# Kernel tuning notes

Hardware: AMD Instinct MI355X
Metric: run time of the kernel (lower is better)

Reference implementation:

```python
import jax, jax.numpy as jnp
import numpy as np

EMBED = 1024
HEAD = 64

def setup_inputs() -> dict:
    key = jax.random.key(0)
    k1, k2, k3, k4 = jax.random.split(key, 4)
    x = jax.random.normal(k1, (8, 2048, EMBED), dtype=jnp.float32)
    # nn.Linear(E, H, bias=False) weights, stored as [E, H] for x @ W
    W_k = jax.random.normal(k2, (EMBED, HEAD), dtype=jnp.float32) * (EMBED ** -0.5)
    W_q = jax.random.normal(k3, (EMBED, HEAD), dtype=jnp.float32) * (EMBED ** -0.5)
    W_v = jax.random.normal(k4, (EMBED, HEAD), dtype=jnp.float32) * (EMBED ** -0.5)
    return {"x": x, "W_k": W_k, "W_q": W_q, "W_v": W_v}

def reference(x, W_k, W_q, W_v):
    B, T, E = x.shape
    keys = jnp.einsum('bte,eh->bth', x, W_k)
    queries = jnp.einsum('bte,eh->bth', x, W_q)
    values = jnp.einsum('bte,eh->bth', x, W_v)
    # NOTE: original scales by embedding size E, not head size
    scores = jnp.einsum('bqh,bkh->bqk', queries, keys) * (E ** -0.5)
    causal = jnp.tril(jnp.ones((T, T), dtype=bool))
    scores = jnp.where(causal, scores, -jnp.inf)
    weights = jax.nn.softmax(scores, axis=-1)
    return jnp.einsum('bqk,bkh->bqh', weights, values)
```

## Files before the change

kernel.cpp:

```cpp
#include <hip/hip_runtime.h>

typedef __attribute__((ext_vector_type(8))) short bf16x8;
typedef __attribute__((ext_vector_type(4))) float f32x4;
typedef __attribute__((ext_vector_type(4))) unsigned short u16x4;
typedef __attribute__((ext_vector_type(8))) unsigned short u16x8;
typedef __attribute__((ext_vector_type(4))) unsigned int u32x4;

#define MFMA(a, b, c) __builtin_amdgcn_mfma_f32_16x16x32_bf16(a, b, c, 0, 0, 0)

static __device__ __forceinline__ unsigned short f2bf(float x) {
    union { float f; unsigned u; } v; v.f = x;
    unsigned r = v.u + 0x7fffu + ((v.u >> 16) & 1u);
    return (unsigned short)(r >> 16);
}

static __device__ __forceinline__ bf16x8 pack_pa(
    float ea0, float ea1, float ea2, float ea3,
    float eb0, float eb1, float eb2, float eb3, bool odd)
{
    unsigned a1, a2, b1, b2;
    asm("v_cvt_pk_bf16_f32 %0, %1, %2" : "=v"(a1) : "v"(ea0), "v"(ea1));
    asm("v_cvt_pk_bf16_f32 %0, %1, %2" : "=v"(a2) : "v"(ea2), "v"(ea3));
    asm("v_cvt_pk_bf16_f32 %0, %1, %2" : "=v"(b1) : "v"(eb0), "v"(eb1));
    asm("v_cvt_pk_bf16_f32 %0, %1, %2" : "=v"(b2) : "v"(eb2), "v"(eb3));
    asm("v_permlane32_swap_b32 %0, %1" : "+v"(a1), "+v"(b1));
    asm("v_permlane32_swap_b32 %0, %1" : "+v"(a2), "+v"(b2));
    int sa1 = __shfl_xor((int)a1, 16);
    int sa2 = __shfl_xor((int)a2, 16);
    int sb1 = __shfl_xor((int)b1, 16);
    int sb2 = __shfl_xor((int)b2, 16);
    u32x4 paw;
    paw[0] = odd ? (unsigned)sb1 : a1;
    paw[1] = odd ? (unsigned)sb2 : a2;
    paw[2] = odd ? b1 : (unsigned)sa1;
    paw[3] = odd ? b2 : (unsigned)sa2;
    return __builtin_bit_cast(bf16x8, paw);
}

__global__ __launch_bounds__(256) void wtrans_k(
    const float* __restrict__ Wk, const float* __restrict__ Wq,
    const float* __restrict__ Wv, unsigned short* __restrict__ Wt)
{
    __shared__ float tl[64][65];
    const int w = blockIdx.x >> 4, kt = blockIdx.x & 15;
    const float* W = (w == 0) ? Wk : (w == 1) ? Wq : Wv;
    const int tid = threadIdx.x;
#pragma unroll
    for (int rep = 0; rep < 4; rep++) {
        int flat = rep * 256 + tid;
        int rr = flat >> 4, c4 = (flat & 15) * 4;
        f32x4 v = *(const f32x4*)(W + (kt * 64 + rr) * 64 + c4);
#pragma unroll
        for (int jj = 0; jj < 4; jj++) tl[c4 + jj][rr] = v[jj];
    }
    __syncthreads();
#pragma unroll
    for (int rep = 0; rep < 2; rep++) {
        int flat = rep * 256 + tid;
        int n = flat >> 3, k8 = (flat & 7) * 8;
        u16x8 h;
#pragma unroll
        for (int jj = 0; jj < 8; jj++) h[jj] = f2bf(tl[n][k8 + jj]);
        *(u16x8*)(Wt + w * 65536 + n * 1024 + kt * 64 + k8) = h;
    }
}

__global__ __launch_bounds__(256) void qkv_k(
    const float* __restrict__ x, const unsigned short* __restrict__ Wt,
    unsigned short* __restrict__ Qb, unsigned short* __restrict__ Kb,
    unsigned short* __restrict__ Vt)
{
    __shared__ __align__(16) unsigned short xl[2][64][72];
    __shared__ __align__(16) unsigned short wl[2][192][72];
    const int tid = threadIdx.x;
    const int wid = tid >> 6, lane = tid & 63;
    const int lrow = lane & 15, g = lane >> 4;
    const int mbase = blockIdx.x * 64;
    const int msrow = (wid & 1) * 32;
    const int ntbase = (wid >> 1) * 6;

    const int xrow = tid >> 2, xc16 = (tid & 3) * 16;
    const int wrow = tid >> 3, wc8 = (tid & 7) * 8;

    f32x4 acc0[6], acc1[6];
#pragma unroll
    for (int j = 0; j < 6; j++) {
        acc0[j] = (f32x4){0.f, 0.f, 0.f, 0.f};
        acc1[j] = (f32x4){0.f, 0.f, 0.f, 0.f};
    }

    f32x4 vx0, vx1, vx2, vx3;
    u16x8 rw0, rw1, rw2, rw3, rw4, rw5;
    {
        const float* xs = x + (mbase + xrow) * 1024 + xc16;
        vx0 = *(const f32x4*)(xs);      vx1 = *(const f32x4*)(xs + 4);
        vx2 = *(const f32x4*)(xs + 8);  vx3 = *(const f32x4*)(xs + 12);
        const unsigned short* ws = Wt + wrow * 1024 + wc8;
        rw0 = *(const u16x8*)(ws);
        rw1 = *(const u16x8*)(ws + 32 * 1024);
        rw2 = *(const u16x8*)(ws + 64 * 1024);
        rw3 = *(const u16x8*)(ws + 96 * 1024);
        rw4 = *(const u16x8*)(ws + 128 * 1024);
        rw5 = *(const u16x8*)(ws + 160 * 1024);
    }

#pragma unroll 1
    for (int t = 0; t < 16; ++t) {
        const int buf = t & 1;
        {
            unsigned d0, d1, d2, d3, d4, d5, d6, d7;
            asm("v_cvt_pk_bf16_f32 %0, %1, %2" : "=v"(d0) : "v"(vx0[0]), "v"(vx0[1]));
            asm("v_cvt_pk_bf16_f32 %0, %1, %2" : "=v"(d1) : "v"(vx0[2]), "v"(vx0[3]));
            asm("v_cvt_pk_bf16_f32 %0, %1, %2" : "=v"(d2) : "v"(vx1[0]), "v"(vx1[1]));
            asm("v_cvt_pk_bf16_f32 %0, %1, %2" : "=v"(d3) : "v"(vx1[2]), "v"(vx1[3]));
            asm("v_cvt_pk_bf16_f32 %0, %1, %2" : "=v"(d4) : "v"(vx2[0]), "v"(vx2[1]));
            asm("v_cvt_pk_bf16_f32 %0, %1, %2" : "=v"(d5) : "v"(vx2[2]), "v"(vx2[3]));
            asm("v_cvt_pk_bf16_f32 %0, %1, %2" : "=v"(d6) : "v"(vx3[0]), "v"(vx3[1]));
            asm("v_cvt_pk_bf16_f32 %0, %1, %2" : "=v"(d7) : "v"(vx3[2]), "v"(vx3[3]));
            u32x4 pk0; pk0[0] = d0; pk0[1] = d1; pk0[2] = d2; pk0[3] = d3;
            u32x4 pk1; pk1[0] = d4; pk1[1] = d5; pk1[2] = d6; pk1[3] = d7;
            *(u32x4*)&xl[buf][xrow][xc16]     = pk0;
            *(u32x4*)&xl[buf][xrow][xc16 + 8] = pk1;
            *(u16x8*)&wl[buf][wrow][wc8]        = rw0;
            *(u16x8*)&wl[buf][wrow + 32][wc8]   = rw1;
            *(u16x8*)&wl[buf][wrow + 64][wc8]   = rw2;
            *(u16x8*)&wl[buf][wrow + 96][wc8]   = rw3;
            *(u16x8*)&wl[buf][wrow + 128][wc8]  = rw4;
            *(u16x8*)&wl[buf][wrow + 160][wc8]  = rw5;
        }
        if (t < 15) {
            const int kc = (t + 1) * 64;
            const float* xs = x + (mbase + xrow) * 1024 + kc + xc16;
            vx0 = *(const f32x4*)(xs);      vx1 = *(const f32x4*)(xs + 4);
            vx2 = *(const f32x4*)(xs + 8);  vx3 = *(const f32x4*)(xs + 12);
            const unsigned short* ws = Wt + wrow * 1024 + kc + wc8;
            rw0 = *(const u16x8*)(ws);
            rw1 = *(const u16x8*)(ws + 32 * 1024);
            rw2 = *(const u16x8*)(ws + 64 * 1024);
            rw3 = *(const u16x8*)(ws + 96 * 1024);
            rw4 = *(const u16x8*)(ws + 128 * 1024);
            rw5 = *(const u16x8*)(ws + 160 * 1024);
        }
        __syncthreads();
#pragma unroll
        for (int ks = 0; ks < 2; ks++) {
            bf16x8 a0 = *(const bf16x8*)&xl[buf][msrow + lrow][ks * 32 + g * 8];
            bf16x8 a1 = *(const bf16x8*)&xl[buf][msrow + 16 + lrow][ks * 32 + g * 8];
#pragma unroll
            for (int j = 0; j < 6; j++) {
                bf16x8 b = *(const bf16x8*)&wl[buf][(ntbase + j) * 16 + lrow][ks * 32 + g * 8];
                acc0[j] = MFMA(a0, b, acc0[j]);
                acc1[j] = MFMA(a1, b, acc1[j]);
            }
        }
    }

#pragma unroll
    for (int j = 0; j < 6; j++) {
        int nt = ntbase + j;
        int w = nt >> 2;
        int col = (nt & 3) * 16 + lrow;
#pragma unroll
        for (int ms = 0; ms < 2; ms++) {
            const f32x4& a = ms ? acc1[j] : acc0[j];
            int r0 = mbase + msrow + ms * 16 + g * 4;
            if (w == 2) {
                int b = r0 >> 11, tt = r0 & 2047;
                u16x4 pv;
                pv[0] = f2bf(a[0]); pv[1] = f2bf(a[1]);
                pv[2] = f2bf(a[2]); pv[3] = f2bf(a[3]);
                *(u16x4*)(Vt + b * 131072 + col * 2048 + tt) = pv;
            } else {
                unsigned short* dst = (w == 0) ? Kb : Qb;
#pragma unroll
                for (int i = 0; i < 4; i++)
                    dst[(r0 + i) * 64 + col] = f2bf(a[i]);
            }
        }
    }
}

__global__ __launch_bounds__(256) void attn_k(
    const unsigned short* __restrict__ Qb, const unsigned short* __restrict__ Kb,
    const unsigned short* __restrict__ Vt, float* __restrict__ pO,
    float* __restrict__ pL)
{
    __shared__ __align__(16) unsigned short klds[2][64][64];
    __shared__ __align__(16) unsigned short vlds[2][64][64];
    const int tid = threadIdx.x;
    const int w = tid >> 6, lane = tid & 63;
    const int lrow = lane & 15, g = lane >> 4;
    const int bid = blockIdx.x;
    const int bandIdx = bid >> 5;
    const int batch = (bid >> 2) & 7;
    const int j = bid & 3;
    const int B = (bandIdx < 16) ? (31 - bandIdx) : (bandIdx - 16);

    const int qb  = B * 64;
    const int nch = B + 1;
    const int nc  = (nch > j) ? ((nch - j + 3) >> 2) : 0;

    const unsigned short* Kbase = Kb + batch * 2048 * 64;
    const unsigned short* Vbase = Vt + batch * 131072;
    const float C2 = 0.03125f * 1.44269504088896f;

    const int sr = tid >> 2;
    const int sc32 = tid & 3;
    const int sb0 = sr * 128 + (((sc32 * 2)     ^ (sr & 7)) << 4);
    const int sb1 = sr * 128 + (((sc32 * 2 + 1) ^ (sr & 7)) << 4);

    const int swz = (lrow & 7) << 4;
    const int rb0 = (lrow) * 128, rb1 = (16 + lrow) * 128,
              rb2 = (32 + lrow) * 128, rb3 = (48 + lrow) * 128;
    const int gk0 = (g << 4) ^ swz;
    const int gk1 = ((4 + g) << 4) ^ swz;
    const bool odd = (g & 1);

    const unsigned short* Qrow = Qb + (batch * 2048 + qb + w * 16 + lrow) * 64;
    bf16x8 q0 = *(const bf16x8*)(Qrow + g * 8);
    bf16x8 q1 = *(const bf16x8*)(Qrow + 32 + g * 8);
    const int qglob = qb + w * 16 + lrow;

    f32x4 o0 = {0.f,0.f,0.f,0.f}, o1 = o0, o2 = o0, o3 = o0;
    float lsum = 0.f;

    u16x8 rk0 = {}, rk1 = {}, rv0 = {}, rv1 = {};
    if (nc > 0) {
        const int kvb = j * 64;
        const unsigned short* ksrc = Kbase + (kvb + sr) * 64 + sc32 * 16;
        rk0 = *(const u16x8*)(ksrc); rk1 = *(const u16x8*)(ksrc + 8);
        const unsigned short* vsrc = Vbase + sr * 2048 + kvb + sc32 * 16;
        rv0 = *(const u16x8*)(vsrc); rv1 = *(const u16x8*)(vsrc + 8);
        char* kb = (char*)&klds[0][0][0];
        char* vb = (char*)&vlds[0][0][0];
        *(u16x8*)(kb + sb0) = rk0; *(u16x8*)(kb + sb1) = rk1;
        *(u16x8*)(vb + sb0) = rv0; *(u16x8*)(vb + sb1) = rv1;
    }
    __syncthreads();

    for (int idx = 0; idx < nc; ++idx) {
        const int c = j + idx * 4;
        const int cur = idx & 1;
        const int kvbase = c * 64;
        if (idx + 1 < nc) {
            const int kvb = kvbase + 256;
            const unsigned short* ksrc = Kbase + (kvb + sr) * 64 + sc32 * 16;
            rk0 = *(const u16x8*)(ksrc); rk1 = *(const u16x8*)(ksrc + 8);
            const unsigned short* vsrc = Vbase + sr * 2048 + kvb + sc32 * 16;
            rv0 = *(const u16x8*)(vsrc); rv1 = *(const u16x8*)(vsrc + 8);
        }

        const char* kb = (const char*)&klds[cur][0][0];
        const char* vb = (const char*)&vlds[cur][0][0];

        f32x4 t0 = {0.f,0.f,0.f,0.f}, t1 = t0, t2 = t0, t3 = t0;
        {
            bf16x8 a;
            a = *(const bf16x8*)(kb + rb0 + gk0); t0 = MFMA(a, q0, t0);
            a = *(const bf16x8*)(kb + rb0 + gk1); t0 = MFMA(a, q1, t0);
            a = *(const bf16x8*)(kb + rb1 + gk0); t1 = MFMA(a, q0, t1);
            a = *(const bf16x8*)(kb + rb1 + gk1); t1 = MFMA(a, q1, t1);
            a = *(const bf16x8*)(kb + rb2 + gk0); t2 = MFMA(a, q0, t2);
            a = *(const bf16x8*)(kb + rb2 + gk1); t2 = MFMA(a, q1, t2);
            a = *(const bf16x8*)(kb + rb3 + gk0); t3 = MFMA(a, q0, t3);
            a = *(const bf16x8*)(kb + rb3 + gk1); t3 = MFMA(a, q1, t3);
        }

        const bool maskc = (c == nch - 1);
        float eA[4], eB[4], eC[4], eD[4];
#pragma unroll
        for (int u = 0; u < 4; u++) {
            float v0 = t0[u] * C2, v1 = t1[u] * C2,
                  v2 = t2[u] * C2, v3 = t3[u] * C2;
            if (maskc) {
                int kvr = kvbase + g * 4 + u;
                v0 = (kvr      > qglob) ? -INFINITY : v0;
                v1 = (kvr + 16 > qglob) ? -INFINITY : v1;
                v2 = (kvr + 32 > qglob) ? -INFINITY : v2;
                v3 = (kvr + 48 > qglob) ? -INFINITY : v3;
            }
            eA[u] = __builtin_exp2f(v0);
            eB[u] = __builtin_exp2f(v1);
            eC[u] = __builtin_exp2f(v2);
            eD[u] = __builtin_exp2f(v3);
            lsum += (eA[u] + eB[u]) + (eC[u] + eD[u]);
        }

        bf16x8 pa0 = pack_pa(eA[0],eA[1],eA[2],eA[3], eB[0],eB[1],eB[2],eB[3], odd);
        bf16x8 pa1 = pack_pa(eC[0],eC[1],eC[2],eC[3], eD[0],eD[1],eD[2],eD[3], odd);

        {
            bf16x8 vv;
            vv = *(const bf16x8*)(vb + rb0 + gk0); o0 = MFMA(pa0, vv, o0);
            vv = *(const bf16x8*)(vb + rb0 + gk1); o0 = MFMA(pa1, vv, o0);
            vv = *(const bf16x8*)(vb + rb1 + gk0); o1 = MFMA(pa0, vv, o1);
            vv = *(const bf16x8*)(vb + rb1 + gk1); o1 = MFMA(pa1, vv, o1);
            vv = *(const bf16x8*)(vb + rb2 + gk0); o2 = MFMA(pa0, vv, o2);
            vv = *(const bf16x8*)(vb + rb2 + gk1); o2 = MFMA(pa1, vv, o2);
            vv = *(const bf16x8*)(vb + rb3 + gk0); o3 = MFMA(pa0, vv, o3);
            vv = *(const bf16x8*)(vb + rb3 + gk1); o3 = MFMA(pa1, vv, o3);
        }

        __syncthreads();
        if (idx + 1 < nc) {
            char* kw = (char*)&klds[cur ^ 1][0][0];
            char* vw = (char*)&vlds[cur ^ 1][0][0];
            *(u16x8*)(kw + sb0) = rk0; *(u16x8*)(kw + sb1) = rk1;
            *(u16x8*)(vw + sb0) = rv0; *(u16x8*)(vw + sb1) = rv1;
        }
        __syncthreads();
    }

    const int qrow0 = batch * 2048 + qb + w * 16;
    float* po = pO + ((size_t)j * 16384 + qrow0) * 64;
#pragma unroll
    for (int u = 0; u < 4; u++) {
        int r = (g * 4 + u) * 64;
        po[r +      lrow] = o0[u];
        po[r + 16 + lrow] = o1[u];
        po[r + 32 + lrow] = o2[u];
        po[r + 48 + lrow] = o3[u];
    }
    lsum += __shfl_xor(lsum, 16);
    lsum += __shfl_xor(lsum, 32);
    if (lane < 16) pL[j * 16384 + qrow0 + lane] = lsum;
}

__global__ __launch_bounds__(256) void comb_k(
    const float* __restrict__ pO, const float* __restrict__ pL,
    float* __restrict__ out)
{
    const int J = 16384 * 64;
    int id = blockIdx.x * 256 + threadIdx.x;
    int row = id >> 2, q = (id & 3) * 16;
    float inv = 1.f / (pL[row] + pL[16384 + row] + pL[32768 + row] + pL[49152 + row]);
    const float* p0 = pO + row * 64 + q;
    float* op = out + row * 64 + q;
#pragma unroll
    for (int k = 0; k < 4; k++) {
        f32x4 s = *(const f32x4*)(p0 + 4 * k)
                + *(const f32x4*)(p0 + J + 4 * k)
                + *(const f32x4*)(p0 + 2 * J + 4 * k)
                + *(const f32x4*)(p0 + 3 * J + 4 * k);
        *(f32x4*)(op + 4 * k) = s * inv;
    }
}

extern "C" void kernel_launch(void* const* d_in, const int* in_sizes, int n_in,
                              void* d_out, int out_size, void* d_ws, size_t ws_size,
                              hipStream_t stream) {
    const float* x  = (const float*)d_in[0];
    const float* Wk = (const float*)d_in[1];
    const float* Wq = (const float*)d_in[2];
    const float* Wv = (const float*)d_in[3];
    float* out = (float*)d_out;

    unsigned short* Wt = (unsigned short*)d_ws;
    unsigned short* Kb = Wt + 3 * 65536;
    unsigned short* Qb = Kb + 16384 * 64;
    unsigned short* Vt = Qb + 16384 * 64;
    float* pO = (float*)(Vt + 131072 * 8);
    float* pL = pO + 4 * 16384 * 64;

    wtrans_k<<<48, 256, 0, stream>>>(Wk, Wq, Wv, Wt);
    qkv_k<<<256, 256, 0, stream>>>(x, Wt, Qb, Kb, Vt);
    attn_k<<<1024, 256, 0, stream>>>(Qb, Kb, Vt, pO, pL);
    comb_k<<<256, 256, 0, stream>>>(pO, pL, out);
}
```

Measured before the change: 47.26 us.

## Pre-tile and XOR-swizzle bf16 weights for contiguous loads in QKV projection

The weight preprocessing kernel now writes the transposed bf16 weights in k-tile-major order, with an XOR swizzle of 16-byte chunks within each 64-element row. The QKV GEMM can then fetch each weight tile as one contiguous block and store it to shared memory without padding. Its MFMA B-fragment reads apply the matching swizzle to avoid bank conflicts. The x tile loads are also reorganized so that 16 threads cover one row's 64 floats, which gives fully coalesced global reads, at the cost of narrower 8-byte LDS stores.

```diff
diff --git a/kernel.cpp b/kernel.cpp
--- a/kernel.cpp
+++ b/kernel.cpp
@@ -61,7 +61,9 @@
         u16x8 h;
 #pragma unroll
         for (int jj = 0; jj < 8; jj++) h[jj] = f2bf(tl[n][k8 + jj]);
-        *(u16x8*)(Wt + w * 65536 + n * 1024 + kt * 64 + k8) = h;
+        int grow = w * 64 + n;
+        int gr = (k8 >> 3) ^ (grow & 7);
+        *(u16x8*)(Wt + kt * 12288 + grow * 64 + gr * 8) = h;
     }
 }
 
@@ -71,7 +73,7 @@
     unsigned short* __restrict__ Vt)
 {
     __shared__ __align__(16) unsigned short xl[2][64][72];
-    __shared__ __align__(16) unsigned short wl[2][192][72];
+    __shared__ __align__(16) unsigned short wl[2][12288];
     const int tid = threadIdx.x;
     const int wid = tid >> 6, lane = tid & 63;
     const int lrow = lane & 15, g = lane >> 4;
@@ -79,8 +81,12 @@
     const int msrow = (wid & 1) * 32;
     const int ntbase = (wid >> 1) * 6;
 
-    const int xrow = tid >> 2, xc16 = (tid & 3) * 16;
-    const int wrow = tid >> 3, wc8 = (tid & 7) * 8;
+    const int xr0 = tid >> 4;
+    const int xc16 = (tid & 15) * 4;
+    const int wofs = tid * 8;
+
+    const int swz0 = ((g    ) ^ (lrow & 7)) << 3;
+    const int swz1 = ((g + 4) ^ (lrow & 7)) << 3;
 
     f32x4 acc0[6], acc1[6];
 #pragma unroll
@@ -92,63 +98,71 @@
     f32x4 vx0, vx1, vx2, vx3;
     u16x8 rw0, rw1, rw2, rw3, rw4, rw5;
     {
-        const float* xs = x + (mbase + xrow) * 1024 + xc16;
-        vx0 = *(const f32x4*)(xs);      vx1 = *(const f32x4*)(xs + 4);
-        vx2 = *(const f32x4*)(xs + 8);  vx3 = *(const f32x4*)(xs + 12);
-        const unsigned short* ws = Wt + wrow * 1024 + wc8;
+        const float* xs = x + mbase * 1024 + xc16;
+        vx0 = *(const f32x4*)(xs + (xr0     ) * 1024);
+        vx1 = *(const f32x4*)(xs + (xr0 + 16) * 1024);
+        vx2 = *(const f32x4*)(xs + (xr0 + 32) * 1024);
+        vx3 = *(const f32x4*)(xs + (xr0 + 48) * 1024);
+        const unsigned short* ws = Wt + wofs;
         rw0 = *(const u16x8*)(ws);
-        rw1 = *(const u16x8*)(ws + 32 * 1024);
-        rw2 = *(const u16x8*)(ws + 64 * 1024);
-        rw3 = *(const u16x8*)(ws + 96 * 1024);
-        rw4 = *(const u16x8*)(ws + 128 * 1024);
-        rw5 = *(const u16x8*)(ws + 160 * 1024);
+        rw1 = *(const u16x8*)(ws + 2048);
+        rw2 = *(const u16x8*)(ws + 4096);
+        rw3 = *(const u16x8*)(ws + 6144);
+        rw4 = *(const u16x8*)(ws + 8192);
+        rw5 = *(const u16x8*)(ws + 10240);
     }
 
 #pragma unroll 1
     for (int t = 0; t < 16; ++t) {
         const int buf = t & 1;
         {
-            unsigned d0, d1, d2, d3, d4, d5, d6, d7;
+            unsigned d0, d1;
+            unsigned* p;
             asm("v_cvt_pk_bf16_f32 %0, %1, %2" : "=v"(d0) : "v"(vx0[0]), "v"(vx0[1]));
             asm("v_cvt_pk_bf16_f32 %0, %1, %2" : "=v"(d1) : "v"(vx0[2]), "v"(vx0[3]));
-            asm("v_cvt_pk_bf16_f32 %0, %1, %2" : "=v"(d2) : "v"(vx1[0]), "v"(vx1[1]));
-            asm("v_cvt_pk_bf16_f32 %0, %1, %2" : "=v"(d3) : "v"(vx1[2]), "v"(vx1[3]));
-            asm("v_cvt_pk_bf16_f32 %0, %1, %2" : "=v"(d4) : "v"(vx2[0]), "v"(vx2[1]));
-            asm("v_cvt_pk_bf16_f32 %0, %1, %2" : "=v"(d5) : "v"(vx2[2]), "v"(vx2[3]));
-            asm("v_cvt_pk_bf16_f32 %0, %1, %2" : "=v"(d6) : "v"(vx3[0]), "v"(vx3[1]));
-            asm("v_cvt_pk_bf16_f32 %0, %1, %2" : "=v"(d7) : "v"(vx3[2]), "v"(vx3[3]));
-            u32x4 pk0; pk0[0] = d0; pk0[1] = d1; pk0[2] = d2; pk0[3] = d3;
-            u32x4 pk1; pk1[0] = d4; pk1[1] = d5; pk1[2] = d6; pk1[3] = d7;
-            *(u32x4*)&xl[buf][xrow][xc16]     = pk0;
-            *(u32x4*)&xl[buf][xrow][xc16 + 8] = pk1;
-            *(u16x8*)&wl[buf][wrow][wc8]        = rw0;
-            *(u16x8*)&wl[buf][wrow + 32][wc8]   = rw1;
-            *(u16x8*)&wl[buf][wrow + 64][wc8]   = rw2;
-            *(u16x8*)&wl[buf][wrow + 96][wc8]   = rw3;
-            *(u16x8*)&wl[buf][wrow + 128][wc8]  = rw4;
-            *(u16x8*)&wl[buf][wrow + 160][wc8]  = rw5;
+            p = (unsigned*)&xl[buf][xr0][xc16];      p[0] = d0; p[1] = d1;
+            asm("v_cvt_pk_bf16_f32 %0, %1, %2" : "=v"(d0) : "v"(vx1[0]), "v"(vx1[1]));
+            asm("v_cvt_pk_bf16_f32 %0, %1, %2" : "=v"(d1) : "v"(vx1[2]), "v"(vx1[3]));
+            p = (unsigned*)&xl[buf][xr0 + 16][xc16]; p[0] = d0; p[1] = d1;
+            asm("v_cvt_pk_bf16_f32 %0, %1, %2" : "=v"(d0) : "v"(vx2[0]), "v"(vx2[1]));
+            asm("v_cvt_pk_bf16_f32 %0, %1, %2" : "=v"(d1) : "v"(vx2[2]), "v"(vx2[3]));
+            p = (unsigned*)&xl[buf][xr0 + 32][xc16]; p[0] = d0; p[1] = d1;
+            asm("v_cvt_pk_bf16_f32 %0, %1, %2" : "=v"(d0) : "v"(vx3[0]), "v"(vx3[1]));
+            asm("v_cvt_pk_bf16_f32 %0, %1, %2" : "=v"(d1) : "v"(vx3[2]), "v"(vx3[3]));
+            p = (unsigned*)&xl[buf][xr0 + 48][xc16]; p[0] = d0; p[1] = d1;
+
+            *(u16x8*)&wl[buf][wofs        ] = rw0;
+            *(u16x8*)&wl[buf][wofs + 2048 ] = rw1;
+            *(u16x8*)&wl[buf][wofs + 4096 ] = rw2;
+            *(u16x8*)&wl[buf][wofs + 6144 ] = rw3;
+            *(u16x8*)&wl[buf][wofs + 8192 ] = rw4;
+            *(u16x8*)&wl[buf][wofs + 10240] = rw5;
         }
         if (t < 15) {
             const int kc = (t + 1) * 64;
-            const float* xs = x + (mbase + xrow) * 1024 + kc + xc16;
-            vx0 = *(const f32x4*)(xs);      vx1 = *(const f32x4*)(xs + 4);
-            vx2 = *(const f32x4*)(xs + 8);  vx3 = *(const f32x4*)(xs + 12);
-            const unsigned short* ws = Wt + wrow * 1024 + kc + wc8;
+            const float* xs = x + mbase * 1024 + kc + xc16;
+            vx0 = *(const f32x4*)(xs + (xr0     ) * 1024);
+            vx1 = *(const f32x4*)(xs + (xr0 + 16) * 1024);
+            vx2 = *(const f32x4*)(xs + (xr0 + 32) * 1024);
+            vx3 = *(const f32x4*)(xs + (xr0 + 48) * 1024);
+            const unsigned short* ws = Wt + (t + 1) * 12288 + wofs;
             rw0 = *(const u16x8*)(ws);
-            rw1 = *(const u16x8*)(ws + 32 * 1024);
-            rw2 = *(const u16x8*)(ws + 64 * 1024);
-            rw3 = *(const u16x8*)(ws + 96 * 1024);
-            rw4 = *(const u16x8*)(ws + 128 * 1024);
-            rw5 = *(const u16x8*)(ws + 160 * 1024);
+            rw1 = *(const u16x8*)(ws + 2048);
+            rw2 = *(const u16x8*)(ws + 4096);
+            rw3 = *(const u16x8*)(ws + 6144);
+            rw4 = *(const u16x8*)(ws + 8192);
+            rw5 = *(const u16x8*)(ws + 10240);
         }
         __syncthreads();
 #pragma unroll
         for (int ks = 0; ks < 2; ks++) {
             bf16x8 a0 = *(const bf16x8*)&xl[buf][msrow + lrow][ks * 32 + g * 8];
             bf16x8 a1 = *(const bf16x8*)&xl[buf][msrow + 16 + lrow][ks * 32 + g * 8];
+            const int swz = ks ? swz1 : swz0;
 #pragma unroll
             for (int j = 0; j < 6; j++) {
-                bf16x8 b = *(const bf16x8*)&wl[buf][(ntbase + j) * 16 + lrow][ks * 32 + g * 8];
+                int row = (ntbase + j) * 16 + lrow;
+                bf16x8 b = *(const bf16x8*)&wl[buf][row * 64 + swz];
                 acc0[j] = MFMA(a0, b, acc0[j]);
                 acc1[j] = MFMA(a1, b, acc1[j]);
             }
```

Result: no change. 46.35 us, median of 2 (-1.9%).
